# Kernel optimization log

Measured on AMD Instinct MI355X. Metric: run time of the kernel, lower is better.

The kernel has to match this reference:

```python
import jax, jax.numpy as jnp
import numpy as np


def setup_inputs() -> dict:
    key = jax.random.key(0)
    ks = jax.random.split(key, 6)
    B, T, D, H = 64, 2048, 128, 256
    stdv = 1.0 / np.sqrt(H)
    return {
        "X": jax.random.normal(ks[0], (B, T, D), dtype=jnp.float32),
        "W": jax.random.normal(ks[1], (D, 4 * H), dtype=jnp.float32) * stdv,
        "U": jax.random.normal(ks[2], (H, 4 * H), dtype=jnp.float32) * stdv,
        "bias": jax.random.normal(ks[3], (4 * H,), dtype=jnp.float32) * stdv,
        "h0": jax.random.normal(ks[4], (B, H), dtype=jnp.float32) * stdv,
        "c0": jax.random.normal(ks[5], (B, H), dtype=jnp.float32) * stdv,
    }


def reference(X, W, U, bias, h0, c0):
    HS = U.shape[0]
    # Hoist input projection into one big GEMM: [B,T,4H]
    xW = jnp.einsum("btd,dg->btg", X, W) + bias

    def step(carry, xw_t):
        h, c = carry
        gates = xw_t + h @ U  # [B,4H]
        i_t = jax.nn.sigmoid(gates[:, :HS])
        f_t = jax.nn.sigmoid(gates[:, HS:2 * HS])
        g_t = jnp.tanh(gates[:, 2 * HS:3 * HS])
        o_t = jax.nn.sigmoid(gates[:, 3 * HS:])
        c_new = f_t * c + i_t * g_t
        h_new = o_t * jnp.tanh(c_new)
        return (h_new, c_new), h_new

    (h_t, c_t), hs = jax.lax.scan(step, (h0, c0), jnp.swapaxes(xW, 0, 1))
    hidden_seq = jnp.swapaxes(hs, 0, 1)  # [B,T,H]
    return (hidden_seq, (h_t, c_t))
```

## Files before the change

### kernel.cpp

```cpp
#include <hip/hip_runtime.h>
#include <hip/hip_bf16.h>

#define BB 64
#define TT 2048
#define DD 128
#define HH 256
#define G4 1024
#define TC 16

typedef _Float16 half2_t __attribute__((ext_vector_type(2)));

#if __has_builtin(__builtin_amdgcn_fdot2)
#define FDOT2(a, b, c) __builtin_amdgcn_fdot2((a), (b), (c), false)
#else
__device__ __forceinline__ float FDOT2(half2_t a, half2_t b, float c) {
    return c + (float)a[0] * (float)b[0] + (float)a[1] * (float)b[1];
}
#endif

__device__ __forceinline__ half2_t u2h(unsigned int u) {
    union { unsigned int u; half2_t h; } x; x.u = u; return x.h;
}
__device__ __forceinline__ unsigned int pkf16(float a, float b) {
    union { _Float16 h[2]; unsigned int u; } x;
    x.h[0] = (_Float16)a; x.h[1] = (_Float16)b; return x.u;
}
__device__ __forceinline__ unsigned short f16b(float a) {
    union { _Float16 h; unsigned short u; } x; x.h = (_Float16)a; return x.u;
}
__device__ __forceinline__ float sigf(float x) {
    return 1.0f / (1.0f + __expf(-x));
}
__device__ __forceinline__ float tanh_fast(float x) {
    return 1.0f - 2.0f / (__expf(2.0f * x) + 1.0f);
}

__global__ void zero_hglob(unsigned long long* hglob) {
    hglob[blockIdx.x * 256 + threadIdx.x] = 0ull;
}

__global__ void __launch_bounds__(128)
pack_slices(const float* __restrict__ src, unsigned short* __restrict__ dst, int K)
{
    const int g = blockIdx.x, kb = blockIdx.y, c = threadIdx.x;
    const int gc = ((c >> 5) << 8) + (g << 5) + (c & 31);
    unsigned int* d32 = (unsigned int*)dst;
    const int dbase = ((g << 7) + c) * K + kb * 64;
    for (int kk = 0; kk < 64; kk += 2) {
        const float a = src[(size_t)(kb * 64 + kk) * G4 + gc];
        const float b = src[(size_t)(kb * 64 + kk + 1) * G4 + gc];
        d32[(dbase + kk) >> 1] = pkf16(a, b);
    }
}

extern "C" __global__ void __launch_bounds__(512, 2)
lstm_pair(const float* __restrict__ X, const unsigned short* __restrict__ Upack,
          const unsigned short* __restrict__ Wpack, const float* __restrict__ bias,
          const float* __restrict__ h0, const float* __restrict__ c0,
          unsigned long long* __restrict__ hglob, float* __restrict__ out)
{
    __shared__ __align__(16) uint4 Ulds4[128 * 32];
    __shared__ __align__(16) uint4 Wlds4[128 * 16];
    __shared__ float xw[2][TC][128];
    __shared__ __align__(16) unsigned short Xs[2 * TC * DD];
    __shared__ float gvp[2][4][128];
    __shared__ __align__(16) unsigned short hsh[2 * HH];

    const int pair = blockIdx.x & 31;
    const int g = blockIdx.x >> 5;
    const int b0 = pair * 2;
    const int tid = threadIdx.x;
    const int wave = tid >> 6, lane = tid & 63;
    const int c = tid & 127, s = tid >> 7;

    {
        const uint4* Usrc = (const uint4*)(Upack + (size_t)g * 32768);
        #pragma unroll
        for (int i = 0; i < 8; ++i) {
            const int idx = i * 512 + tid;
            const int cc = idx >> 5, gr = idx & 31;
            Ulds4[cc * 32 + (gr ^ (cc & 31))] = Usrc[idx];
        }
        const uint4* Wsrc = (const uint4*)(Wpack + (size_t)g * 16384);
        #pragma unroll
        for (int i = 0; i < 4; ++i) {
            const int idx = i * 512 + tid;
            const int cc = idx >> 4, gr = idx & 15;
            Wlds4[cc * 16 + (gr ^ (cc & 15))] = Wsrc[idx];
        }
    }
    hsh[tid] = f16b(h0[(size_t)(b0 + (tid >> 8)) * HH + (tid & 255)]);
    float c_reg = 0.0f, h_last = 0.0f;
    if (wave == 0) {
        const int p = lane >> 5, j = lane & 31;
        c_reg = c0[(size_t)(b0 + p) * HH + (g << 5) + j];
        h_last = h0[(size_t)(b0 + p) * HH + (g << 5) + j];
    }
    const float bc = bias[((c >> 5) << 8) + (g << 5) + (c & 31)];
    __syncthreads();

    for (int chunk = 0; chunk < TT / TC; ++chunk) {
        const int t0 = chunk * TC;

        #pragma unroll
        for (int r = 0; r < 2; ++r) {
            const float4 xv = ((const float4*)(X + ((size_t)(b0 + r) * TT + t0) * DD))[tid];
            ((uint2*)Xs)[r * 512 + tid] = make_uint2(pkf16(xv.x, xv.y), pkf16(xv.z, xv.w));
        }
        __syncthreads();

        {
            const int p = s >> 1, th = s & 1;
            float acc[8];
            #pragma unroll
            for (int t = 0; t < 8; ++t) acc[t] = bc;
            #pragma unroll
            for (int k8 = 0; k8 < 16; ++k8) {
                const uint4 w4 = Wlds4[c * 16 + (k8 ^ (c & 15))];
                #pragma unroll
                for (int t = 0; t < 8; ++t) {
                    const uint4 xg = *(const uint4*)((const char*)Xs +
                                     ((p * 16 + th * 8 + t) << 8) + (k8 << 4));
                    acc[t] = FDOT2(u2h(xg.x), u2h(w4.x), acc[t]);
                    acc[t] = FDOT2(u2h(xg.y), u2h(w4.y), acc[t]);
                    acc[t] = FDOT2(u2h(xg.z), u2h(w4.z), acc[t]);
                    acc[t] = FDOT2(u2h(xg.w), u2h(w4.w), acc[t]);
                }
            }
            #pragma unroll
            for (int t = 0; t < 8; ++t) xw[p][th * 8 + t][c] = acc[t];
        }
        __syncthreads();

        for (int tt2 = 0; tt2 < TC; ++tt2) {
            const int tau = t0 + tt2;

            {
                float a0 = (s == 0) ? xw[0][tt2][c] : 0.0f;
                float a1 = (s == 0) ? xw[1][tt2][c] : 0.0f;
                #pragma unroll
                for (int ii = 0; ii < 8; ++ii) {
                    const uint4 ug = Ulds4[c * 32 + ((s * 8 + ii) ^ (c & 31))];
                    const uint4 hg0 = *(const uint4*)((const char*)hsh + (s << 7) + (ii << 4));
                    const uint4 hg1 = *(const uint4*)((const char*)hsh + 512 + (s << 7) + (ii << 4));
                    a0 = FDOT2(u2h(ug.x), u2h(hg0.x), a0);
                    a1 = FDOT2(u2h(ug.x), u2h(hg1.x), a1);
                    a0 = FDOT2(u2h(ug.y), u2h(hg0.y), a0);
                    a1 = FDOT2(u2h(ug.y), u2h(hg1.y), a1);
                    a0 = FDOT2(u2h(ug.z), u2h(hg0.z), a0);
                    a1 = FDOT2(u2h(ug.z), u2h(hg1.z), a1);
                    a0 = FDOT2(u2h(ug.w), u2h(hg0.w), a0);
                    a1 = FDOT2(u2h(ug.w), u2h(hg1.w), a1);
                }
                gvp[0][s][c] = a0;
                gvp[1][s][c] = a1;
            }
            __syncthreads();

            const int par = (tau + 1) & 1;
            if (wave == 0) {
                const int p = lane >> 5, j = lane & 31;
                const float* gv = &gvp[p][0][0];
                float gi = 0.f, gf = 0.f, gg = 0.f, go = 0.f;
                #pragma unroll
                for (int qs = 0; qs < 4; ++qs) {
                    gi += gv[qs * 128 + j];
                    gf += gv[qs * 128 + 32 + j];
                    gg += gv[qs * 128 + 64 + j];
                    go += gv[qs * 128 + 96 + j];
                }
                const float it = sigf(gi), ft = sigf(gf);
                const float gt = tanh_fast(gg), ot = sigf(go);
                c_reg = fmaf(ft, c_reg, it * gt);
                const float hn = ot * tanh_fast(c_reg);
                h_last = hn;
                const unsigned long long pkt =
                    ((unsigned long long)(unsigned)(tau + 1) << 32) |
                    (unsigned long long)__float_as_uint(hn);
                __hip_atomic_store(&hglob[((((pair << 3) + g) << 1) + par) * 64 + lane],
                                   pkt, __ATOMIC_RELAXED, __HIP_MEMORY_SCOPE_AGENT);
                out[((size_t)(b0 + p) * TT + tau) * HH + (g << 5) + j] = hn;
                hsh[(p << 8) + (g << 5) + j] = f16b(hn);
            } else if (tau < TT - 1) {
                const int pg = (g + wave) & 7;
                const int p = lane >> 5, j = lane & 31;
                const unsigned long long* q =
                    &hglob[((((pair << 3) + pg) << 1) + par) * 64 + lane];
                unsigned long long v;
                int spins = 0;
                do {
                    v = __hip_atomic_load(q, __ATOMIC_RELAXED, __HIP_MEMORY_SCOPE_AGENT);
                    if (++spins > (1 << 20)) break;
                } while ((unsigned)(v >> 32) != (unsigned)(tau + 1));
                hsh[(p << 8) + (pg << 5) + j] = f16b(__uint_as_float((unsigned)v));
            }
            __syncthreads();
        }
    }

    if (wave == 0) {
        const int p = lane >> 5, j = lane & 31;
        const size_t base = (size_t)BB * TT * HH;
        out[base + (size_t)(b0 + p) * HH + (g << 5) + j] = h_last;
        out[base + (size_t)BB * HH + (size_t)(b0 + p) * HH + (g << 5) + j] = c_reg;
    }
}

__global__ void zero_flags(int* flags) {
    flags[blockIdx.x * 256 + threadIdx.x] = 0;
}

__global__ void __launch_bounds__(256)
pack_cols(const float* __restrict__ src, unsigned short* __restrict__ dst, int K)
{
    const int g = blockIdx.x, kb = blockIdx.y, c = threadIdx.x;
    const int gc = ((c >> 6) << 8) + (g << 6) + (c & 63);
    unsigned int* d32 = (unsigned int*)dst;
    const int dbase = ((g << 8) + c) * K + kb * 64;
    for (int kk = 0; kk < 64; kk += 2) {
        const float a = src[(size_t)(kb * 64 + kk) * G4 + gc];
        const float b = src[(size_t)(kb * 64 + kk + 1) * G4 + gc];
        d32[(dbase + kk) >> 1] = pkf16(a, b);
    }
}

extern "C" __global__ void __launch_bounds__(512, 2)
lstm_sync(const float* __restrict__ X, const unsigned short* __restrict__ Upack,
          const unsigned short* __restrict__ Wpack, const float* __restrict__ bias,
          const float* __restrict__ h0, const float* __restrict__ c0,
          unsigned int* __restrict__ hglob, int* __restrict__ flags,
          float* __restrict__ out)
{
    __shared__ uint4 Ulds4[HH * 32];
    __shared__ float xw[TC][256];
    __shared__ __align__(16) unsigned short Xs[TC * DD];
    __shared__ float gvp[2][256];
    __shared__ __align__(16) unsigned short hsh[HH];

    const int b = blockIdx.x & 63;
    const int g = blockIdx.x >> 6;
    const int tid = threadIdx.x;
    const int wave = tid >> 6, lane = tid & 63;
    const int c = tid & 255, s = tid >> 8;
    const int gc = ((c >> 6) << 8) + (g << 6) + (c & 63);
    const int fbase = b * 4;

    {
        const uint4* Usrc = (const uint4*)(Upack + (size_t)g * 65536);
        #pragma unroll
        for (int i = 0; i < 16; ++i) {
            const int idx = i * 512 + tid;
            const int cc = idx >> 5, k8 = idx & 31;
            Ulds4[cc * 32 + (k8 ^ (cc & 31))] = Usrc[idx];
        }
    }
    if (tid < HH) hsh[tid] = f16b(h0[b * HH + tid]);
    float c_reg = 0.0f, h_last = 0.0f;
    if (wave == 0) {
        c_reg = c0[b * HH + (g << 6) + lane];
        h_last = h0[b * HH + (g << 6) + lane];
    }
    const float bc = bias[gc];
    __syncthreads();

    const unsigned short* Wg = Wpack + (size_t)g * 32768;

    for (int chunk = 0; chunk < TT / TC; ++chunk) {
        const int t0 = chunk * TC;
        {
            const float4 xv = ((const float4*)(X + ((size_t)b * TT + t0) * DD))[tid];
            ((uint2*)Xs)[tid] = make_uint2(pkf16(xv.x, xv.y), pkf16(xv.z, xv.w));
        }
        __syncthreads();
        {
            float acc[8];
            #pragma unroll
            for (int t = 0; t < 8; ++t) acc[t] = bc;
            const uint4* Wc = (const uint4*)(Wg + (size_t)c * 128);
            #pragma unroll
            for (int k8 = 0; k8 < 16; ++k8) {
                const uint4 w4 = Wc[k8];
                #pragma unroll
                for (int t = 0; t < 8; ++t) {
                    const uint4 xg = *(const uint4*)((const char*)Xs + (s * 8 + t) * 256 + (k8 << 4));
                    acc[t] = FDOT2(u2h(xg.x), u2h(w4.x), acc[t]);
                    acc[t] = FDOT2(u2h(xg.y), u2h(w4.y), acc[t]);
                    acc[t] = FDOT2(u2h(xg.z), u2h(w4.z), acc[t]);
                    acc[t] = FDOT2(u2h(xg.w), u2h(w4.w), acc[t]);
                }
            }
            #pragma unroll
            for (int t = 0; t < 8; ++t) xw[s * 8 + t][c] = acc[t];
        }
        __syncthreads();

        for (int tt = 0; tt < TC; ++tt) {
            const int tau = t0 + tt;
            {
                float a0 = (s == 0) ? xw[tt][c] : 0.0f;
                float a1 = 0.0f;
                const int kbase = s << 4;
                #pragma unroll
                for (int i = 0; i < 16; ++i) {
                    const int k8 = kbase + i;
                    const uint4 ug = Ulds4[c * 32 + (k8 ^ (c & 31))];
                    const uint4 hg = *(const uint4*)((const char*)hsh + (k8 << 4));
                    a0 = FDOT2(u2h(ug.x), u2h(hg.x), a0);
                    a1 = FDOT2(u2h(ug.y), u2h(hg.y), a1);
                    a0 = FDOT2(u2h(ug.z), u2h(hg.z), a0);
                    a1 = FDOT2(u2h(ug.w), u2h(hg.w), a1);
                }
                gvp[s][c] = a0 + a1;
            }
            __syncthreads();

            const int par = (tau + 1) & 1;
            if (wave == 0) {
                const int j = lane;
                const float gi = gvp[0][j]       + gvp[1][j];
                const float gf = gvp[0][64 + j]  + gvp[1][64 + j];
                const float gg = gvp[0][128 + j] + gvp[1][128 + j];
                const float go = gvp[0][192 + j] + gvp[1][192 + j];
                const float it = sigf(gi), ft = sigf(gf);
                const float gt = tanh_fast(gg), ot = sigf(go);
                c_reg = fmaf(ft, c_reg, it * gt);
                const float hn = ot * tanh_fast(c_reg);
                h_last = hn;
                const float lo = __shfl(hn, 2 * j);
                const float hi = __shfl(hn, 2 * j + 1);
                if (j < 32) {
                    __hip_atomic_store(&hglob[(((fbase + g) << 1) + par) * 32 + j],
                                       pkf16(lo, hi),
                                       __ATOMIC_RELAXED, __HIP_MEMORY_SCOPE_AGENT);
                }
                asm volatile("s_waitcnt vmcnt(0)" ::: "memory");
                if (j == 0) {
                    __hip_atomic_store(&flags[(fbase + g) * 8], tau + 1,
                                       __ATOMIC_RELAXED, __HIP_MEMORY_SCOPE_AGENT);
                }
                out[((size_t)b * TT + tau) * HH + (g << 6) + j] = hn;
                hsh[(g << 6) + j] = f16b(hn);
            } else if (wave <= 3 && tau < TT - 1) {
                const int pg = (g + wave) & 3;
                int spins = 0;
                while (__hip_atomic_load(&flags[(fbase + pg) * 8], __ATOMIC_RELAXED,
                                         __HIP_MEMORY_SCOPE_AGENT) < tau + 1) {
                    if (++spins > (1 << 20)) break;
                }
                if (lane < 32) {
                    const unsigned int pv = __hip_atomic_load(
                        &hglob[(((fbase + pg) << 1) + par) * 32 + lane],
                        __ATOMIC_RELAXED, __HIP_MEMORY_SCOPE_AGENT);
                    ((unsigned int*)hsh)[(pg << 5) + lane] = pv;
                }
            }
            __syncthreads();
        }
    }

    if (wave == 0) {
        const size_t base = (size_t)BB * TT * HH;
        out[base + (size_t)b * HH + (g << 6) + lane] = h_last;
        out[base + (size_t)BB * HH + (size_t)b * HH + (g << 6) + lane] = c_reg;
    }
}

extern "C" __global__ void __launch_bounds__(512)
lstm_persist(const float* __restrict__ X, const float* __restrict__ W,
             const float* __restrict__ U, const float* __restrict__ bias,
             const float* __restrict__ h0, const float* __restrict__ c0,
             float* __restrict__ out)
{
    __shared__ float xw[TC][G4];
    __shared__ float Xs[TC][DD];
    __shared__ float hsh[HH];
    __shared__ float gv[G4];

    const int b = blockIdx.x;
    const int tid = threadIdx.x;
    const float2* __restrict__ U2 = reinterpret_cast<const float2*>(U);
    const float2* __restrict__ W2 = reinterpret_cast<const float2*>(W);

    float c_reg = 0.0f;
    if (tid < HH) { hsh[tid] = h0[b * HH + tid]; c_reg = c0[b * HH + tid]; }
    const float2 bs = reinterpret_cast<const float2*>(bias)[tid];
    __syncthreads();

    for (int chunk = 0; chunk < TT / TC; ++chunk) {
        const int t0 = chunk * TC;
        {
            const float4* src = reinterpret_cast<const float4*>(X + ((size_t)b * TT + t0) * DD);
            float4* dst = reinterpret_cast<float4*>(&Xs[0][0]);
            for (int i = tid; i < TC * DD / 4; i += 512) dst[i] = src[i];
        }
        __syncthreads();
        float acc0[TC], acc1[TC];
        #pragma unroll
        for (int t = 0; t < TC; ++t) { acc0[t] = bs.x; acc1[t] = bs.y; }
        for (int kk = 0; kk < DD; kk += 4) {
            const float2 w0 = W2[(size_t)(kk + 0) * (G4 / 2) + tid];
            const float2 w1 = W2[(size_t)(kk + 1) * (G4 / 2) + tid];
            const float2 w2 = W2[(size_t)(kk + 2) * (G4 / 2) + tid];
            const float2 w3 = W2[(size_t)(kk + 3) * (G4 / 2) + tid];
            #pragma unroll
            for (int t = 0; t < TC; ++t) {
                const float4 xv = *reinterpret_cast<const float4*>(&Xs[t][kk]);
                acc0[t] = fmaf(xv.x, w0.x, acc0[t]); acc1[t] = fmaf(xv.x, w0.y, acc1[t]);
                acc0[t] = fmaf(xv.y, w1.x, acc0[t]); acc1[t] = fmaf(xv.y, w1.y, acc1[t]);
                acc0[t] = fmaf(xv.z, w2.x, acc0[t]); acc1[t] = fmaf(xv.z, w2.y, acc1[t]);
                acc0[t] = fmaf(xv.w, w3.x, acc0[t]); acc1[t] = fmaf(xv.w, w3.y, acc1[t]);
            }
        }
        #pragma unroll
        for (int t = 0; t < TC; ++t)
            *reinterpret_cast<float2*>(&xw[t][2 * tid]) = make_float2(acc0[t], acc1[t]);
        __syncthreads();

        for (int t = 0; t < TC; ++t) {
            const float2 x2 = *reinterpret_cast<const float2*>(&xw[t][2 * tid]);
            float a0 = x2.x, a1 = x2.y;
            #pragma unroll 4
            for (int k = 0; k < HH; k += 4) {
                const float4 hk = *reinterpret_cast<const float4*>(&hsh[k]);
                const float2 u0 = U2[(size_t)(k + 0) * (G4 / 2) + tid];
                const float2 u1 = U2[(size_t)(k + 1) * (G4 / 2) + tid];
                const float2 u2 = U2[(size_t)(k + 2) * (G4 / 2) + tid];
                const float2 u3 = U2[(size_t)(k + 3) * (G4 / 2) + tid];
                a0 = fmaf(hk.x, u0.x, a0); a1 = fmaf(hk.x, u0.y, a1);
                a0 = fmaf(hk.y, u1.x, a0); a1 = fmaf(hk.y, u1.y, a1);
                a0 = fmaf(hk.z, u2.x, a0); a1 = fmaf(hk.z, u2.y, a1);
                a0 = fmaf(hk.w, u3.x, a0); a1 = fmaf(hk.w, u3.y, a1);
            }
            *reinterpret_cast<float2*>(&gv[2 * tid]) = make_float2(a0, a1);
            __syncthreads();
            if (tid < HH) {
                const float it = sigf(gv[tid]);
                const float ft = sigf(gv[tid + HH]);
                const float gt = tanh_fast(gv[tid + 2 * HH]);
                const float ot = sigf(gv[tid + 3 * HH]);
                c_reg = fmaf(ft, c_reg, it * gt);
                const float hn = ot * tanh_fast(c_reg);
                hsh[tid] = hn;
                out[((size_t)b * TT + (t0 + t)) * HH + tid] = hn;
            }
            __syncthreads();
        }
    }
    if (tid < HH) {
        const size_t base = (size_t)BB * TT * HH;
        out[base + (size_t)b * HH + tid] = hsh[tid];
        out[base + (size_t)BB * HH + (size_t)b * HH + tid] = c_reg;
    }
}

extern "C" void kernel_launch(void* const* d_in, const int* in_sizes, int n_in,
                              void* d_out, int out_size, void* d_ws, size_t ws_size,
                              hipStream_t stream) {
    const float* X    = (const float*)d_in[0];
    const float* W    = (const float*)d_in[1];
    const float* U    = (const float*)d_in[2];
    const float* bias = (const float*)d_in[3];
    const float* h0   = (const float*)d_in[4];
    const float* c0   = (const float*)d_in[5];
    float* out = (float*)d_out;
    (void)in_sizes; (void)n_in; (void)out_size;

    const size_t upk6 = 512 * 1024;
    const size_t wpk6 = 256 * 1024;
    const size_t hgl6 = 256 * 1024;
    if (ws_size >= upk6 + wpk6 + hgl6) {
        unsigned short* Upack = (unsigned short*)d_ws;
        unsigned short* Wpack = (unsigned short*)((char*)d_ws + upk6);
        unsigned long long* hglob = (unsigned long long*)((char*)d_ws + upk6 + wpk6);
        zero_hglob<<<dim3(128), dim3(256), 0, stream>>>(hglob);
        pack_slices<<<dim3(8, 4), dim3(128), 0, stream>>>(U, Upack, 256);
        pack_slices<<<dim3(8, 2), dim3(128), 0, stream>>>(W, Wpack, 128);
        lstm_pair<<<dim3(256), dim3(512), 0, stream>>>(
            X, Upack, Wpack, bias, h0, c0, hglob, out);
        return;
    }

    const size_t upk = 512 * 1024;
    const size_t wpk = 256 * 1024;
    const size_t hgl = 64 * 1024;
    const size_t flg = 8 * 1024;
    if (ws_size >= upk + wpk + hgl + flg) {
        unsigned short* Upack = (unsigned short*)d_ws;
        unsigned short* Wpack = (unsigned short*)((char*)d_ws + upk);
        unsigned int*   hglob = (unsigned int*)((char*)d_ws + upk + wpk);
        int*            flags = (int*)((char*)d_ws + upk + wpk + hgl);
        zero_flags<<<dim3(8), dim3(256), 0, stream>>>(flags);
        pack_cols<<<dim3(4, 4), dim3(256), 0, stream>>>(U, Upack, 256);
        pack_cols<<<dim3(4, 2), dim3(256), 0, stream>>>(W, Wpack, 128);
        lstm_sync<<<dim3(256), dim3(512), 0, stream>>>(
            X, Upack, Wpack, bias, h0, c0, hglob, flags, out);
        return;
    }

    lstm_persist<<<dim3(BB), dim3(512), 0, stream>>>(X, W, U, bias, h0, c0, out);
}
```

Baseline: 3.960 ms.

## Interleave two batch rows' recurrence phases to hide cross-block h exchange latency

```diff
diff --git a/kernel.cpp b/kernel.cpp
--- a/kernel.cpp
+++ b/kernel.cpp
@@ -33,6 +33,9 @@
 }
 __device__ __forceinline__ float tanh_fast(float x) {
     return 1.0f - 2.0f / (__expf(2.0f * x) + 1.0f);
+}
+__device__ __forceinline__ void bar_lgkm() {
+    asm volatile("s_waitcnt lgkmcnt(0)\n\ts_barrier" ::: "memory");
 }
 
 __global__ void zero_hglob(unsigned long long* hglob) {
@@ -54,7 +57,7 @@
 }
 
 extern "C" __global__ void __launch_bounds__(512, 2)
-lstm_pair(const float* __restrict__ X, const unsigned short* __restrict__ Upack,
+lstm_pipe(const float* __restrict__ X, const unsigned short* __restrict__ Upack,
           const unsigned short* __restrict__ Wpack, const float* __restrict__ bias,
           const float* __restrict__ h0, const float* __restrict__ c0,
           unsigned long long* __restrict__ hglob, float* __restrict__ out)
@@ -63,7 +66,7 @@
     __shared__ __align__(16) uint4 Wlds4[128 * 16];
     __shared__ float xw[2][TC][128];
     __shared__ __align__(16) unsigned short Xs[2 * TC * DD];
-    __shared__ float gvp[2][4][128];
+    __shared__ float gvp[4][128];
     __shared__ __align__(16) unsigned short hsh[2 * HH];
 
     const int pair = blockIdx.x & 31;
@@ -90,14 +93,19 @@
         }
     }
     hsh[tid] = f16b(h0[(size_t)(b0 + (tid >> 8)) * HH + (tid & 255)]);
-    float c_reg = 0.0f, h_last = 0.0f;
-    if (wave == 0) {
-        const int p = lane >> 5, j = lane & 31;
-        c_reg = c0[(size_t)(b0 + p) * HH + (g << 5) + j];
-        h_last = h0[(size_t)(b0 + p) * HH + (g << 5) + j];
+    float c_reg0 = 0.0f, c_reg1 = 0.0f, h_last0 = 0.0f, h_last1 = 0.0f;
+    if (wave == 0 && lane < 32) {
+        c_reg0 = c0[(size_t)b0 * HH + (g << 5) + lane];
+        c_reg1 = c0[(size_t)(b0 + 1) * HH + (g << 5) + lane];
+        h_last0 = h0[(size_t)b0 * HH + (g << 5) + lane];
+        h_last1 = h0[(size_t)(b0 + 1) * HH + (g << 5) + lane];
     }
     const float bc = bias[((c >> 5) << 8) + (g << 5) + (c & 31)];
     __syncthreads();
+
+    const size_t obase0 = (size_t)b0 * TT * HH + (g << 5);
+    const size_t obase1 = (size_t)(b0 + 1) * TT * HH + (g << 5);
+    const int slotbase = ((pair << 3) + g) << 1;
 
     for (int chunk = 0; chunk < TT / TC; ++chunk) {
         const int t0 = chunk * TC;
@@ -107,7 +115,7 @@
             const float4 xv = ((const float4*)(X + ((size_t)(b0 + r) * TT + t0) * DD))[tid];
             ((uint2*)Xs)[r * 512 + tid] = make_uint2(pkf16(xv.x, xv.y), pkf16(xv.z, xv.w));
         }
-        __syncthreads();
+        bar_lgkm();
 
         {
             const int p = s >> 1, th = s & 1;
@@ -130,79 +138,119 @@
             #pragma unroll
             for (int t = 0; t < 8; ++t) xw[p][th * 8 + t][c] = acc[t];
         }
-        __syncthreads();
+        bar_lgkm();
 
         for (int tt2 = 0; tt2 < TC; ++tt2) {
             const int tau = t0 + tt2;
 
             {
-                float a0 = (s == 0) ? xw[0][tt2][c] : 0.0f;
-                float a1 = (s == 0) ? xw[1][tt2][c] : 0.0f;
+                float a = (s == 0) ? xw[0][tt2][c] : 0.0f;
                 #pragma unroll
                 for (int ii = 0; ii < 8; ++ii) {
                     const uint4 ug = Ulds4[c * 32 + ((s * 8 + ii) ^ (c & 31))];
-                    const uint4 hg0 = *(const uint4*)((const char*)hsh + (s << 7) + (ii << 4));
-                    const uint4 hg1 = *(const uint4*)((const char*)hsh + 512 + (s << 7) + (ii << 4));
-                    a0 = FDOT2(u2h(ug.x), u2h(hg0.x), a0);
-                    a1 = FDOT2(u2h(ug.x), u2h(hg1.x), a1);
-                    a0 = FDOT2(u2h(ug.y), u2h(hg0.y), a0);
-                    a1 = FDOT2(u2h(ug.y), u2h(hg1.y), a1);
-                    a0 = FDOT2(u2h(ug.z), u2h(hg0.z), a0);
-                    a1 = FDOT2(u2h(ug.z), u2h(hg1.z), a1);
-                    a0 = FDOT2(u2h(ug.w), u2h(hg0.w), a0);
-                    a1 = FDOT2(u2h(ug.w), u2h(hg1.w), a1);
-                }
-                gvp[0][s][c] = a0;
-                gvp[1][s][c] = a1;
-            }
-            __syncthreads();
-
-            const int par = (tau + 1) & 1;
+                    const uint4 hg = *(const uint4*)((const char*)hsh + (s << 7) + (ii << 4));
+                    a = FDOT2(u2h(ug.x), u2h(hg.x), a);
+                    a = FDOT2(u2h(ug.y), u2h(hg.y), a);
+                    a = FDOT2(u2h(ug.z), u2h(hg.z), a);
+                    a = FDOT2(u2h(ug.w), u2h(hg.w), a);
+                }
+                gvp[s][c] = a;
+            }
+            bar_lgkm();
+
             if (wave == 0) {
-                const int p = lane >> 5, j = lane & 31;
-                const float* gv = &gvp[p][0][0];
-                float gi = 0.f, gf = 0.f, gg = 0.f, go = 0.f;
+                if (lane < 32) {
+                    const int j = lane;
+                    float gi = 0.f, gf = 0.f, gg = 0.f, go = 0.f;
+                    #pragma unroll
+                    for (int q = 0; q < 4; ++q) {
+                        gi += gvp[q][j];       gf += gvp[q][32 + j];
+                        gg += gvp[q][64 + j];  go += gvp[q][96 + j];
+                    }
+                    const float it = sigf(gi), ft = sigf(gf);
+                    const float gt = tanh_fast(gg), ot = sigf(go);
+                    c_reg0 = fmaf(ft, c_reg0, it * gt);
+                    const float hn = ot * tanh_fast(c_reg0);
+                    h_last0 = hn;
+                    const unsigned long long pkt =
+                        ((unsigned long long)(unsigned)(tau + 1) << 32) |
+                        (unsigned long long)__float_as_uint(hn);
+                    __hip_atomic_store(&hglob[(size_t)(slotbase + ((tau + 1) & 1)) * 64 + j],
+                                       pkt, __ATOMIC_RELAXED, __HIP_MEMORY_SCOPE_AGENT);
+                    out[obase0 + (size_t)tau * HH + j] = hn;
+                    hsh[(g << 5) + j] = f16b(hn);
+                }
+            } else if (tau >= 1 && lane < 32) {
+                const int pg = (g + wave) & 7;
+                const unsigned long long* q =
+                    &hglob[(size_t)((((pair << 3) + pg) << 1) + (tau & 1)) * 64 + 32 + lane];
+                unsigned long long v; int spins = 0;
+                do {
+                    v = __hip_atomic_load(q, __ATOMIC_RELAXED, __HIP_MEMORY_SCOPE_AGENT);
+                    if (++spins > (1 << 20)) break;
+                } while ((unsigned)(v >> 32) != (unsigned)tau);
+                hsh[256 + (pg << 5) + lane] = f16b(__uint_as_float((unsigned)v));
+            }
+            bar_lgkm();
+
+            {
+                float a = (s == 0) ? xw[1][tt2][c] : 0.0f;
                 #pragma unroll
-                for (int qs = 0; qs < 4; ++qs) {
-                    gi += gv[qs * 128 + j];
-                    gf += gv[qs * 128 + 32 + j];
-                    gg += gv[qs * 128 + 64 + j];
-                    go += gv[qs * 128 + 96 + j];
-                }
-                const float it = sigf(gi), ft = sigf(gf);
-                const float gt = tanh_fast(gg), ot = sigf(go);
-                c_reg = fmaf(ft, c_reg, it * gt);
-                const float hn = ot * tanh_fast(c_reg);
-                h_last = hn;
-                const unsigned long long pkt =
-                    ((unsigned long long)(unsigned)(tau + 1) << 32) |
-                    (unsigned long long)__float_as_uint(hn);
-                __hip_atomic_store(&hglob[((((pair << 3) + g) << 1) + par) * 64 + lane],
-                                   pkt, __ATOMIC_RELAXED, __HIP_MEMORY_SCOPE_AGENT);
-                out[((size_t)(b0 + p) * TT + tau) * HH + (g << 5) + j] = hn;
-                hsh[(p << 8) + (g << 5) + j] = f16b(hn);
-            } else if (tau < TT - 1) {
+                for (int ii = 0; ii < 8; ++ii) {
+                    const uint4 ug = Ulds4[c * 32 + ((s * 8 + ii) ^ (c & 31))];
+                    const uint4 hg = *(const uint4*)((const char*)hsh + 512 + (s << 7) + (ii << 4));
+                    a = FDOT2(u2h(ug.x), u2h(hg.x), a);
+                    a = FDOT2(u2h(ug.y), u2h(hg.y), a);
+                    a = FDOT2(u2h(ug.z), u2h(hg.z), a);
+                    a = FDOT2(u2h(ug.w), u2h(hg.w), a);
+                }
+                gvp[s][c] = a;
+            }
+            bar_lgkm();
+
+            if (wave == 0) {
+                if (lane < 32) {
+                    const int j = lane;
+                    float gi = 0.f, gf = 0.f, gg = 0.f, go = 0.f;
+                    #pragma unroll
+                    for (int q = 0; q < 4; ++q) {
+                        gi += gvp[q][j];       gf += gvp[q][32 + j];
+                        gg += gvp[q][64 + j];  go += gvp[q][96 + j];
+                    }
+                    const float it = sigf(gi), ft = sigf(gf);
+                    const float gt = tanh_fast(gg), ot = sigf(go);
+                    c_reg1 = fmaf(ft, c_reg1, it * gt);
+                    const float hn = ot * tanh_fast(c_reg1);
+                    h_last1 = hn;
+                    const unsigned long long pkt =
+                        ((unsigned long long)(unsigned)(tau + 1) << 32) |
+                        (unsigned long long)__float_as_uint(hn);
+                    __hip_atomic_store(&hglob[(size_t)(slotbase + ((tau + 1) & 1)) * 64 + 32 + j],
+                                       pkt, __ATOMIC_RELAXED, __HIP_MEMORY_SCOPE_AGENT);
+                    out[obase1 + (size_t)tau * HH + j] = hn;
+                    hsh[256 + (g << 5) + j] = f16b(hn);
+                }
+            } else if (tau < TT - 1 && lane < 32) {
                 const int pg = (g + wave) & 7;
-                const int p = lane >> 5, j = lane & 31;
                 const unsigned long long* q =
-                    &hglob[((((pair << 3) + pg) << 1) + par) * 64 + lane];
-                unsigned long long v;
-                int spins = 0;
+                    &hglob[(size_t)((((pair << 3) + pg) << 1) + ((tau + 1) & 1)) * 64 + lane];
+                unsigned long long v; int spins = 0;
                 do {
                     v = __hip_atomic_load(q, __ATOMIC_RELAXED, __HIP_MEMORY_SCOPE_AGENT);
                     if (++spins > (1 << 20)) break;
                 } while ((unsigned)(v >> 32) != (unsigned)(tau + 1));
-                hsh[(p << 8) + (pg << 5) + j] = f16b(__uint_as_float((unsigned)v));
-            }
-            __syncthreads();
-        }
-    }
-
-    if (wave == 0) {
-        const int p = lane >> 5, j = lane & 31;
+                hsh[(pg << 5) + lane] = f16b(__uint_as_float((unsigned)v));
+            }
+            bar_lgkm();
+        }
+    }
+
+    if (wave == 0 && lane < 32) {
         const size_t base = (size_t)BB * TT * HH;
-        out[base + (size_t)(b0 + p) * HH + (g << 5) + j] = h_last;
-        out[base + (size_t)BB * HH + (size_t)(b0 + p) * HH + (g << 5) + j] = c_reg;
+        out[base + (size_t)b0 * HH + (g << 5) + lane] = h_last0;
+        out[base + (size_t)(b0 + 1) * HH + (g << 5) + lane] = h_last1;
+        out[base + (size_t)BB * HH + (size_t)b0 * HH + (g << 5) + lane] = c_reg0;
+        out[base + (size_t)BB * HH + (size_t)(b0 + 1) * HH + (g << 5) + lane] = c_reg1;
     }
 }
 
@@ -465,17 +513,17 @@
     float* out = (float*)d_out;
     (void)in_sizes; (void)n_in; (void)out_size;
 
-    const size_t upk6 = 512 * 1024;
-    const size_t wpk6 = 256 * 1024;
-    const size_t hgl6 = 256 * 1024;
-    if (ws_size >= upk6 + wpk6 + hgl6) {
+    const size_t upk7 = 512 * 1024;
+    const size_t wpk7 = 256 * 1024;
+    const size_t hgl7 = 256 * 1024;
+    if (ws_size >= upk7 + wpk7 + hgl7) {
         unsigned short* Upack = (unsigned short*)d_ws;
-        unsigned short* Wpack = (unsigned short*)((char*)d_ws + upk6);
-        unsigned long long* hglob = (unsigned long long*)((char*)d_ws + upk6 + wpk6);
+        unsigned short* Wpack = (unsigned short*)((char*)d_ws + upk7);
+        unsigned long long* hglob = (unsigned long long*)((char*)d_ws + upk7 + wpk7);
         zero_hglob<<<dim3(128), dim3(256), 0, stream>>>(hglob);
         pack_slices<<<dim3(8, 4), dim3(128), 0, stream>>>(U, Upack, 256);
         pack_slices<<<dim3(8, 2), dim3(128), 0, stream>>>(W, Wpack, 128);
-        lstm_pair<<<dim3(256), dim3(512), 0, stream>>>(
+        lstm_pipe<<<dim3(256), dim3(512), 0, stream>>>(
             X, Upack, Wpack, bias, h0, c0, hglob, out);
         return;
     }
```

New measurement: 3.553 ms. 10.3% less time.
